# Performance work log

Hardware: AMD Instinct MI355X
Metric: run time of the kernel (lower is better)

## Reference

```python
import jax, jax.numpy as jnp
import numpy as np

B, K, H, W = 16, 32, 28, 28   # batch, set size, image h, image w
HID, OUT = 64, 64             # hid_dim, out_dim
NOPS = 8                      # permutation-equivariant 3->3 pool/broadcast basis ops


def setup_inputs() -> dict:
    key = jax.random.key(0)
    ks = jax.random.split(key, 8)
    def p(k, shape, fan_in):
        return jax.random.normal(k, shape, jnp.float32) / np.float32(np.sqrt(fan_in))
    return dict(
        x=jax.random.normal(ks[0], (B, K, H, W), jnp.float32),
        conv1_w=p(ks[1], (32, 1, 3, 3), 9),
        conv1_b=jnp.zeros((32,), jnp.float32),
        conv2_w=p(ks[2], (64, 32, 3, 3), 32 * 9),
        conv2_b=jnp.zeros((64,), jnp.float32),
        fc_w=p(ks[3], (HID, 64 * 7 * 7), 64 * 7 * 7),
        fc_b=jnp.zeros((HID,), jnp.float32),
        eq_w=p(ks[4], (HID, OUT, NOPS), HID * NOPS),
        eq_b=jnp.zeros((OUT,), jnp.float32),
        out_w=p(ks[5], (1, OUT), OUT),
        out_b=jnp.zeros((1,), jnp.float32),
    )


def _conv2d(x, w, b):
    y = jax.lax.conv_general_dilated(x, w, (1, 1), 'SAME',
                                     dimension_numbers=('NCHW', 'OIHW', 'NCHW'))
    return y + b[None, :, None, None]


def _maxpool2(x):
    return jax.lax.reduce_window(x, -jnp.inf, jax.lax.max,
                                 (1, 1, 2, 2), (1, 1, 2, 2), 'VALID')


def _forward(x, conv1_w, conv1_b, conv2_w, conv2_b, fc_w, fc_b, eq_w, eq_b, out_w, out_b):
    # --- BasicConvNet embed: (B*K, 1, H, W) -> (B*K, HID) ---
    x1 = x.reshape(B * K, 1, H, W)
    h1 = _maxpool2(jax.nn.relu(_conv2d(x1, conv1_w, conv1_b)))   # (B*K, 32, 14, 14)
    h2 = _maxpool2(jax.nn.relu(_conv2d(h1, conv2_w, conv2_b)))   # (B*K, 64, 7, 7)
    feat = jax.nn.relu(h2.reshape(B * K, -1) @ fc_w.T + fc_b)    # (B*K, HID)
    x4 = feat.reshape(B, K, HID)

    # --- triple outer product: (B, HID, K, K, K), no contracted index ---
    x5 = jnp.einsum('bid,bjd,bkd->bdijk', x4, x4, x4)

    # --- SetEq3to3: 8 equivariant pool/broadcast basis ops, contracted with eq_w[d,e,o].
    # Contract each pooled tensor with its slice of eq_w BEFORE broadcasting (same math,
    # avoids materializing 8 full (B,d,K,K,K) op tensors). ---
    m_i  = x5.mean(2)           # (B, d, j, k)
    m_j  = x5.mean(3)           # (B, d, i, k)
    m_k  = x5.mean(4)           # (B, d, i, j)
    m_ij = m_i.mean(2)          # (B, d, k)
    m_ik = m_i.mean(3)          # (B, d, j)
    m_jk = m_j.mean(3)          # (B, d, i)
    m_all = m_ij.mean(2)        # (B, d)

    x6 = (jnp.einsum('bdijk,de->beijk', x5, eq_w[:, :, 0])
          + jnp.einsum('bdjk,de->bejk', m_i, eq_w[:, :, 1])[:, :, None, :, :]
          + jnp.einsum('bdik,de->beik', m_j, eq_w[:, :, 2])[:, :, :, None, :]
          + jnp.einsum('bdij,de->beij', m_k, eq_w[:, :, 3])[:, :, :, :, None]
          + jnp.einsum('bdk,de->bek', m_ij, eq_w[:, :, 4])[:, :, None, None, :]
          + jnp.einsum('bdj,de->bej', m_ik, eq_w[:, :, 5])[:, :, None, :, None]
          + jnp.einsum('bdi,de->bei', m_jk, eq_w[:, :, 6])[:, :, :, None, None]
          + jnp.einsum('bd,de->be', m_all, eq_w[:, :, 7])[:, :, None, None, None]
          + eq_b[None, :, None, None, None])          # (B, OUT, K, K, K)

    # permute to channels-last, relu, pool over (i,j,k), relu, final linear
    x7 = jax.nn.relu(x6.transpose(0, 2, 3, 4, 1))     # (B, K, K, K, OUT)
    x8 = x7.mean(axis=(1, 2, 3))                      # (B, OUT)
    x9 = jax.nn.relu(x8)
    # dropout_prob = 0 -> identity
    return x9 @ out_w.T + out_b                       # (B, 1)


def reference(x, conv1_w, conv1_b, conv2_w, conv2_b, fc_w, fc_b, eq_w, eq_b, out_w, out_b):
    return _forward(x, conv1_w, conv1_b, conv2_w, conv2_b, fc_w, fc_b,
                    eq_w, eq_b, out_w, out_b)
```

## Files before the change

kernel.cpp:

```cpp
#include <hip/hip_runtime.h>
#include <hip/hip_bf16.h>


typedef __attribute__((ext_vector_type(8))) short short8;
typedef __attribute__((ext_vector_type(4))) float f32x4;

__device__ __forceinline__ f32x4 mfma_bf16(short8 a, short8 b, f32x4 c) {
  return __builtin_amdgcn_mfma_f32_16x16x32_bf16(a, b, c, 0, 0, 0);
}

__device__ __forceinline__ unsigned short f2bs(float f) {
  unsigned int u = __float_as_uint(f);
  unsigned int r = u + 0x7fffu + ((u >> 16) & 1u);
  return (unsigned short)(r >> 16);
}
__device__ __forceinline__ unsigned int pk2(float x, float y) {
  union { __hip_bfloat162 h; unsigned int u; } cv;
  cv.h = __float22bfloat162_rn(make_float2(x, y));
  return cv.u;
}
__device__ __forceinline__ void stb4(short* p, float4 v) {
  *(unsigned int*)(p)     = pk2(v.x, v.y);
  *(unsigned int*)(p + 2) = pk2(v.z, v.w);
}

__global__ __launch_bounds__(256) void k1_conv1(const float* __restrict__ x,
    const float* __restrict__ w, const float* __restrict__ bias,
    short* __restrict__ h1b,
    const float* __restrict__ eqw, float* __restrict__ Wt,
    const float* __restrict__ fcw, short* __restrict__ fcwb) {
  const int n = blockIdx.x, t = threadIdx.x;
  if (n >= 512) {
    if (n < 520) {
      const int m = n - 512;
      for (int idx = t; idx < 4096; idx += 256) {
        int e = idx >> 6, d = idx & 63;
        Wt[m*4096 + idx] = eqw[d*512 + e*8 + m];
      }
    } else {
      int base = (n - 520)*12544 + t;
      for (int q = 0; q < 49; ++q) {
        int idx = base + q*256;
        fcwb[idx] = (short)f2bs(fcw[idx]);
      }
    }
    return;
  }
  __shared__ float si[30*30];
  __shared__ float sw[32*9];
  __shared__ float sb[32];
  for (int idx = t; idx < 900; idx += 256) si[idx] = 0.f;
  for (int idx = t; idx < 288; idx += 256) sw[idx] = w[idx];
  if (t < 32) sb[t] = bias[t];
  __syncthreads();
  for (int idx = t; idx < 784; idx += 256) {
    int y = idx / 28, xx = idx - y*28;
    si[(y+1)*30 + xx + 1] = x[n*784 + idx];
  }
  __syncthreads();
  for (int idx = t; idx < 6272; idx += 256) {
    int pos = idx >> 5, c = idx & 31;
    int py = pos / 14, px = pos - py*14;
    float pt[4][4];
#pragma unroll
    for (int r = 0; r < 4; ++r)
#pragma unroll
      for (int q = 0; q < 4; ++q)
        pt[r][q] = si[(2*py + r)*30 + 2*px + q];
    const float* wc = &sw[c*9];
    float w0=wc[0], w1=wc[1], w2=wc[2], w3=wc[3], w4=wc[4], w5=wc[5], w6=wc[6], w7=wc[7], w8=wc[8];
    float bb = sb[c];
    float best = 0.f;
#pragma unroll
    for (int a = 0; a < 2; ++a)
#pragma unroll
      for (int b2 = 0; b2 < 2; ++b2) {
        float v = bb
          + w0*pt[a+0][b2+0] + w1*pt[a+0][b2+1] + w2*pt[a+0][b2+2]
          + w3*pt[a+1][b2+0] + w4*pt[a+1][b2+1] + w5*pt[a+1][b2+2]
          + w6*pt[a+2][b2+0] + w7*pt[a+2][b2+1] + w8*pt[a+2][b2+2];
        best = fmaxf(best, v);
      }
    h1b[n*6272 + idx] = (short)f2bs(best);
  }
}

__global__ __launch_bounds__(256, 2) void k2_mfma(const short* __restrict__ h1b,
    const float* __restrict__ w, const float* __restrict__ bias,
    short* __restrict__ h2b) {
  __shared__ __align__(16) short inT[16*18*40];
  const int n = blockIdx.x, t = threadIdx.x;
  const int wv = t >> 6, l = t & 63, quad = l >> 4, col = l & 15;

  unsigned int* zp = (unsigned int*)inT;
  for (int idx = t; idx < 16*18*20; idx += 256) zp[idx] = 0u;

  const int c_out = wv*16 + col;
  float w72[72];
  {
    const float4* src = (const float4*)(w + c_out*288 + quad*72);
#pragma unroll
    for (int q = 0; q < 18; ++q) {
      float4 v = src[q];
      w72[q*4+0] = v.x; w72[q*4+1] = v.y; w72[q*4+2] = v.z; w72[q*4+3] = v.w;
    }
  }
  union SU { short8 v; unsigned int u[4]; };
  short8 Bq[9];
#pragma unroll
  for (int dd = 0; dd < 9; ++dd) {
    SU b;
#pragma unroll
    for (int q = 0; q < 4; ++q)
      b.u[q] = pk2(w72[(2*q)*9 + dd], w72[(2*q+1)*9 + dd]);
    Bq[dd] = b.v;
  }
  const float bb = bias[c_out];
  __syncthreads();

  {
    const uint4* src = (const uint4*)(h1b + n*6272);
    for (int idx = t; idx < 784; idx += 256) {
      uint4 v = src[idx];
      int pos = idx >> 2, cb = (idx & 3) * 8;
      int y = pos / 14, xx = pos - y*14;
      *(uint4*)&inT[(y+1)*720 + (xx+1)*40 + cb] = v;
    }
  }
  __syncthreads();

  for (int p = 0; p < 7; ++p) {
    short8 Ar[4][3];
#pragma unroll
    for (int rr = 0; rr < 4; ++rr)
#pragma unroll
      for (int dx = 0; dx < 3; ++dx)
        Ar[rr][dx] = *(const short8*)&inT[(2*p + rr)*720 + (col + dx)*40 + quad*8];
    f32x4 a0 = {0.f,0.f,0.f,0.f}, a1 = {0.f,0.f,0.f,0.f};
#pragma unroll
    for (int dy = 0; dy < 3; ++dy)
#pragma unroll
      for (int dx = 0; dx < 3; ++dx) {
        a0 = mfma_bf16(Ar[dy][dx],     Bq[dy*3 + dx], a0);
        a1 = mfma_bf16(Ar[dy + 1][dx], Bq[dy*3 + dx], a1);
      }
#pragma unroll
    for (int a = 0; a < 2; ++a) {
      int px = quad*2 + a;
      if (px < 7) {
        float m0 = fmaxf(fmaxf(a0[2*a], a0[2*a + 1]), fmaxf(a1[2*a], a1[2*a + 1]));
        h2b[n*3136 + c_out*49 + p*7 + px] = (short)f2bs(fmaxf(m0 + bb, 0.f));
      }
    }
  }
}

__global__ __launch_bounds__(256) void k3_mfma(const short* __restrict__ h2b,
    const short* __restrict__ fcwb, float* __restrict__ part) {
  const int blk = blockIdx.x, kp = blockIdx.y, t = threadIdx.x;
  const int w = t >> 6, l = t & 63, quad = l >> 4, col = l & 15;
  const int mt = w & 1, nh = w >> 1;
  const int img = blk*32 + mt*16 + col;
  const short* Ap = h2b + img*3136 + kp*224 + quad*8;
  const short* B0 = fcwb + (nh*32 + col)*3136 + kp*224 + quad*8;
  const short* B1 = fcwb + (nh*32 + 16 + col)*3136 + kp*224 + quad*8;
  f32x4 acc0 = {0.f,0.f,0.f,0.f}, acc1 = {0.f,0.f,0.f,0.f};
#pragma unroll
  for (int q = 0; q < 7; ++q) {
    short8 A  = *(const short8*)(Ap + q*32);
    short8 b0 = *(const short8*)(B0 + q*32);
    short8 b1 = *(const short8*)(B1 + q*32);
    acc0 = mfma_bf16(A, b0, acc0);
    acc1 = mfma_bf16(A, b1, acc1);
  }
  const int e0 = nh*32 + col, e1 = e0 + 16;
  const int base = blk*32 + mt*16 + quad*4;
  float* dst = part + kp*32768;
#pragma unroll
  for (int r = 0; r < 4; ++r) {
    dst[(base + r)*64 + e0] = acc0[r];
    dst[(base + r)*64 + e1] = acc1[r];
  }
}

__global__ __launch_bounds__(256) void k4_prep(const float* __restrict__ part,
    const float* __restrict__ fb, const float* __restrict__ Wt,
    const float* __restrict__ eqb, float* __restrict__ feat,
    float* __restrict__ s, float* __restrict__ t7c, float* __restrict__ x8) {
  __shared__ __align__(16) float sf[2048];
  __shared__ float ss[64];
  const int b = blockIdx.x, t = threadIdx.x;
  for (int v4 = t; v4 < 512; v4 += 256) {
    float4 a = {0.f, 0.f, 0.f, 0.f};
#pragma unroll
    for (int kp = 0; kp < 14; ++kp) {
      float4 p = *(const float4*)&part[kp*32768 + b*2048 + v4*4];
      a.x += p.x; a.y += p.y; a.z += p.z; a.w += p.w;
    }
    float4 fbv = *(const float4*)&fb[(v4*4) & 63];
    float4 r;
    r.x = fmaxf(a.x + fbv.x, 0.f);
    r.y = fmaxf(a.y + fbv.y, 0.f);
    r.z = fmaxf(a.z + fbv.z, 0.f);
    r.w = fmaxf(a.w + fbv.w, 0.f);
    *(float4*)&sf[v4*4] = r;
    *(float4*)&feat[b*2048 + v4*4] = r;
  }
  __syncthreads();
  if (t < 64) {
    float a = 0.f;
    for (int i = 0; i < 32; ++i) a += sf[i*64 + t];
    a *= (1.f/32.f);
    s[b*64 + t] = a;
    ss[t] = a;
  }
  __syncthreads();
  if (t < 64) {
    const float* W7 = Wt + 7*4096 + t*64;
    float t7 = 0.f;
    for (int d = 0; d < 64; ++d) {
      float sv = ss[d];
      t7 += sv*sv*sv * W7[d];
    }
    t7c[b*64 + t] = t7 + eqb[t];
    x8[b*64 + t] = 0.f;
  }
}

__global__ __launch_bounds__(256, 2) void k5_mfma(const float* __restrict__ feat,
    const float* __restrict__ s_, const float* __restrict__ Wt,
    const float* __restrict__ t7c, float* __restrict__ x8) {
  __shared__ __align__(16) float Fm[32*68];
  __shared__ __align__(16) float FI[64];
  __shared__ __align__(16) float SV[64];
  __shared__ __align__(16) float C0[64];
  __shared__ float C0P[128];
  __shared__ float KCf[32*68];
  __shared__ float JCf[32*68];
  __shared__ float RED[256];
  __shared__ __align__(16) short Fb[32*72];
  __shared__ __align__(16) short QPb[64*72];
  __shared__ __align__(16) short G2b[64*72];
  __shared__ __align__(16) short G3b[64*72];

  const int i = blockIdx.x, b = blockIdx.y, t = threadIdx.x;
  const int w = t >> 6, l = t & 63, quad = l >> 4, col = l & 15;

  for (int idx = t; idx < 2048; idx += 256) {
    int r = idx >> 6, d = idx & 63;
    float v = feat[b*2048 + idx];
    Fm[r*68 + d] = v;
    Fb[r*72 + d] = (short)f2bs(v);
  }
  if (t < 64) { FI[t] = feat[b*2048 + i*64 + t]; SV[t] = s_[b*64 + t]; }
  __syncthreads();

  {
    const int e = t >> 2, dbase = (t & 3) * 16;
    const float* W0 = Wt + 0*4096 + e*64;
    const float* W1 = Wt + 1*4096 + e*64;
    const float* W2 = Wt + 2*4096 + e*64;
    const float* W3 = Wt + 3*4096 + e*64;
    const float* W4 = Wt + 4*4096 + e*64;
    const float* W5 = Wt + 5*4096 + e*64;
#pragma unroll
    for (int q = 0; q < 4; ++q) {
      int off = dbase + q*4;
      float4 fi4 = *(const float4*)&FI[off];
      float4 sv4 = *(const float4*)&SV[off];
      float4 w0 = *(const float4*)&W0[off];
      float4 w1 = *(const float4*)&W1[off];
      float4 w2 = *(const float4*)&W2[off];
      float4 w3 = *(const float4*)&W3[off];
      float4 w4 = *(const float4*)&W4[off];
      float4 w5 = *(const float4*)&W5[off];
      float4 qp = fi4*w0 + sv4*w1;
      float4 g2 = sv4*(fi4*w2 + sv4*w4);
      float4 g3 = sv4*(fi4*w3 + sv4*w5);
      stb4(&QPb[e*72 + off], qp);
      stb4(&G2b[e*72 + off], g2);
      stb4(&G3b[e*72 + off], g3);
    }
  }
  if (t < 128) {
    int e = t & 63, dh = t >> 6;
    const float* W6 = Wt + 6*4096 + e*64 + dh*32;
    const float* fip = FI + dh*32;
    const float* svp = SV + dh*32;
    float a = 0.f;
#pragma unroll
    for (int dd = 0; dd < 32; ++dd) {
      float sd = svp[dd];
      a += sd*sd*fip[dd]*W6[dd];
    }
    C0P[dh*64 + e] = a;
  }
  __syncthreads();

  if (w < 2) {
    const short* G = w ? G3b : G2b;
    float* DST = w ? JCf : KCf;
    short8 Bf[4][2];
#pragma unroll
    for (int n = 0; n < 4; ++n)
#pragma unroll
      for (int s2 = 0; s2 < 2; ++s2)
        Bf[n][s2] = *(const short8*)&G[(n*16 + col)*72 + s2*32 + quad*8];
#pragma unroll
    for (int m = 0; m < 2; ++m) {
      short8 A0 = *(const short8*)&Fb[(m*16 + col)*72 + quad*8];
      short8 A1 = *(const short8*)&Fb[(m*16 + col)*72 + 32 + quad*8];
#pragma unroll
      for (int n = 0; n < 4; ++n) {
        f32x4 z = {0.f, 0.f, 0.f, 0.f};
        f32x4 ac = mfma_bf16(A1, Bf[n][1], mfma_bf16(A0, Bf[n][0], z));
#pragma unroll
        for (int r = 0; r < 4; ++r)
          DST[(m*16 + quad*4 + r)*68 + n*16 + col] = ac[r];
      }
    }
  } else if (w == 2) {
    C0[l] = C0P[l] + C0P[64 + l] + t7c[b*64 + l];
  }
  __syncthreads();

  float c0v[4];
#pragma unroll
  for (int n = 0; n < 4; ++n) c0v[n] = C0[n*16 + col];
  float jcq[8][4];
#pragma unroll
  for (int jj = 0; jj < 8; ++jj)
#pragma unroll
    for (int n = 0; n < 4; ++n)
      jcq[jj][n] = JCf[(w*8 + jj)*68 + n*16 + col] + c0v[n];
  float kcv[2][4][4];
#pragma unroll
  for (int kb2 = 0; kb2 < 2; ++kb2)
#pragma unroll
    for (int r = 0; r < 4; ++r)
#pragma unroll
      for (int n = 0; n < 4; ++n)
        kcv[kb2][r][n] = KCf[(kb2*16 + quad*4 + r)*68 + n*16 + col];
  short8 Bq[4][2];
#pragma unroll
  for (int n = 0; n < 4; ++n)
#pragma unroll
    for (int s2 = 0; s2 < 2; ++s2)
      Bq[n][s2] = *(const short8*)&QPb[(n*16 + col)*72 + s2*32 + quad*8];

  float4 fkv[2][4];
#pragma unroll
  for (int kb2 = 0; kb2 < 2; ++kb2) {
    const float* fk = &Fm[(kb2*16 + col)*68 + quad*8];
    fkv[kb2][0] = *(const float4*)(fk);
    fkv[kb2][1] = *(const float4*)(fk + 4);
    fkv[kb2][2] = *(const float4*)(fk + 32);
    fkv[kb2][3] = *(const float4*)(fk + 36);
  }

  float sum[4] = {0.f, 0.f, 0.f, 0.f};
  union SU { short8 v; unsigned int u[4]; };

#pragma unroll
  for (int jj = 0; jj < 8; ++jj) {
    const float* fj = &Fm[(w*8 + jj)*68 + quad*8];
    float4 j0 = *(const float4*)(fj);
    float4 j1 = *(const float4*)(fj + 4);
    float4 j2 = *(const float4*)(fj + 32);
    float4 j3 = *(const float4*)(fj + 36);
#pragma unroll
    for (int kb2 = 0; kb2 < 2; ++kb2) {
      float4 k0 = fkv[kb2][0], k1 = fkv[kb2][1];
      float4 k2v = fkv[kb2][2], k3v = fkv[kb2][3];
      SU A0, A1;
      A0.u[0] = pk2(j0.x*k0.x, j0.y*k0.y);
      A0.u[1] = pk2(j0.z*k0.z, j0.w*k0.w);
      A0.u[2] = pk2(j1.x*k1.x, j1.y*k1.y);
      A0.u[3] = pk2(j1.z*k1.z, j1.w*k1.w);
      A1.u[0] = pk2(j2.x*k2v.x, j2.y*k2v.y);
      A1.u[1] = pk2(j2.z*k2v.z, j2.w*k2v.w);
      A1.u[2] = pk2(j3.x*k3v.x, j3.y*k3v.y);
      A1.u[3] = pk2(j3.z*k3v.z, j3.w*k3v.w);
      f32x4 ac[4];
#pragma unroll
      for (int n = 0; n < 4; ++n) {
        f32x4 z = {0.f, 0.f, 0.f, 0.f};
        ac[n] = mfma_bf16(A1.v, Bq[n][1], mfma_bf16(A0.v, Bq[n][0], z));
      }
#pragma unroll
      for (int n = 0; n < 4; ++n)
#pragma unroll
        for (int r = 0; r < 4; ++r) {
          float v = ac[n][r] + kcv[kb2][r][n] + jcq[jj][n];
          sum[n] += fmaxf(v, 0.f);
        }
    }
  }

#pragma unroll
  for (int n = 0; n < 4; ++n) {
    float v = sum[n];
    v += __shfl_xor(v, 16, 64);
    v += __shfl_xor(v, 32, 64);
    if (l < 16) RED[w*64 + n*16 + l] = v;
  }
  __syncthreads();
  if (t < 64) {
    float tot = RED[t] + RED[64 + t] + RED[128 + t] + RED[192 + t];
    atomicAdd(&x8[b*64 + t], tot);
  }
}

__global__ __launch_bounds__(64) void k6_out(const float* __restrict__ x8,
    const float* __restrict__ ow, const float* __restrict__ ob,
    float* __restrict__ out) {
  const int bb = blockIdx.x, t = threadIdx.x;
  float v = fmaxf(x8[bb*64 + t] * (1.f/32768.f), 0.f) * ow[t];
#pragma unroll
  for (int off = 32; off > 0; off >>= 1) v += __shfl_down(v, off, 64);
  if (t == 0) out[bb] = v + ob[0];
}

extern "C" void kernel_launch(void* const* d_in, const int* in_sizes, int n_in,
                              void* d_out, int out_size, void* d_ws, size_t ws_size,
                              hipStream_t stream) {
  const float* x   = (const float*)d_in[0];
  const float* c1w = (const float*)d_in[1];
  const float* c1b = (const float*)d_in[2];
  const float* c2w = (const float*)d_in[3];
  const float* c2b = (const float*)d_in[4];
  const float* fcw = (const float*)d_in[5];
  const float* fcb = (const float*)d_in[6];
  const float* eqw = (const float*)d_in[7];
  const float* eqb = (const float*)d_in[8];
  const float* ow  = (const float*)d_in[9];
  const float* ob  = (const float*)d_in[10];
  float* out = (float*)d_out;

  short* h1b  = (short*)d_ws;
  short* h2b  = h1b + 512*6272;
  float* feat = (float*)(h2b + 512*3136);
  float* s    = feat + 512*64;
  float* t7c  = s + 1024;
  float* x8   = t7c + 1024;
  float* Wt   = x8 + 1024;
  short* fcwb = (short*)(Wt + 32768);
  float* part = (float*)(fcwb + 200704);

  hipLaunchKernelGGL(k1_conv1, dim3(536), dim3(256), 0, stream,
                     x, c1w, c1b, h1b, eqw, Wt, fcw, fcwb);
  hipLaunchKernelGGL(k2_mfma,  dim3(512), dim3(256), 0, stream, h1b, c2w, c2b, h2b);
  hipLaunchKernelGGL(k3_mfma,  dim3(16, 14), dim3(256), 0, stream, h2b, fcwb, part);
  hipLaunchKernelGGL(k4_prep,  dim3(16),  dim3(256), 0, stream,
                     part, fcb, Wt, eqb, feat, s, t7c, x8);
  hipLaunchKernelGGL(k5_mfma,  dim3(32, 16), dim3(256), 0, stream, feat, s, Wt, t7c, x8);
  hipLaunchKernelGGL(k6_out,   dim3(16),  dim3(64),  0, stream, x8, ow, ob, out);
}
```

Baseline: 131.5 us.

## Fuse conv1 into conv2 kernel and fold output head into k5 via last-block counter

Conv1+relu+pool is computed directly into the shared-memory padded bf16 tile that conv2's MFMA loop reads, so the h1 intermediate no longer goes to global memory and one launch disappears. Conv1 is restructured so each thread computes 4 channels for one pooled position, with weights held in registers and a packed 8-byte shared store. The final output-head kernel is removed: k5 blocks bump a per-batch counter after their atomics, and the last block applies relu and the output linear layer. In exchange the fused kernel carries more registers and shared memory, which may lower occupancy, and the head now depends on the atomic counter and fences.

```diff
diff --git a/kernel.cpp b/kernel.cpp
--- a/kernel.cpp
+++ b/kernel.cpp
@@ -24,9 +24,10 @@
   *(unsigned int*)(p + 2) = pk2(v.z, v.w);
 }
 
-__global__ __launch_bounds__(256) void k1_conv1(const float* __restrict__ x,
-    const float* __restrict__ w, const float* __restrict__ bias,
-    short* __restrict__ h1b,
+__global__ __launch_bounds__(256, 2) void k12_conv(const float* __restrict__ x,
+    const float* __restrict__ w1, const float* __restrict__ b1,
+    const float* __restrict__ w2, const float* __restrict__ b2,
+    short* __restrict__ h2b,
     const float* __restrict__ eqw, float* __restrict__ Wt,
     const float* __restrict__ fcw, short* __restrict__ fcwb) {
   const int n = blockIdx.x, t = threadIdx.x;
@@ -49,82 +50,83 @@
   __shared__ float si[30*30];
   __shared__ float sw[32*9];
   __shared__ float sb[32];
+  __shared__ __align__(16) short inT[16*18*40];
+  const int wv = t >> 6, l = t & 63, quad = l >> 4, col = l & 15;
+
+  const int c_out = wv*16 + col;
+  float w72[72];
+  {
+    const float4* src = (const float4*)(w2 + c_out*288 + quad*72);
+#pragma unroll
+    for (int q = 0; q < 18; ++q) {
+      float4 v = src[q];
+      w72[q*4+0] = v.x; w72[q*4+1] = v.y; w72[q*4+2] = v.z; w72[q*4+3] = v.w;
+    }
+  }
+  union SU { short8 v; unsigned int u[4]; };
+  short8 Bq[9];
+#pragma unroll
+  for (int dd = 0; dd < 9; ++dd) {
+    SU b;
+#pragma unroll
+    for (int q = 0; q < 4; ++q)
+      b.u[q] = pk2(w72[(2*q)*9 + dd], w72[(2*q+1)*9 + dd]);
+    Bq[dd] = b.v;
+  }
+  const float bb2 = b2[c_out];
+
   for (int idx = t; idx < 900; idx += 256) si[idx] = 0.f;
-  for (int idx = t; idx < 288; idx += 256) sw[idx] = w[idx];
-  if (t < 32) sb[t] = bias[t];
+  {
+    unsigned int* zp = (unsigned int*)inT;
+    for (int idx = t; idx < 5760; idx += 256) zp[idx] = 0u;
+  }
+  for (int idx = t; idx < 288; idx += 256) sw[idx] = w1[idx];
+  if (t < 32) sb[t] = b1[t];
   __syncthreads();
   for (int idx = t; idx < 784; idx += 256) {
     int y = idx / 28, xx = idx - y*28;
     si[(y+1)*30 + xx + 1] = x[n*784 + idx];
   }
   __syncthreads();
-  for (int idx = t; idx < 6272; idx += 256) {
-    int pos = idx >> 5, c = idx & 31;
-    int py = pos / 14, px = pos - py*14;
-    float pt[4][4];
-#pragma unroll
-    for (int r = 0; r < 4; ++r)
-#pragma unroll
-      for (int q = 0; q < 4; ++q)
-        pt[r][q] = si[(2*py + r)*30 + 2*px + q];
-    const float* wc = &sw[c*9];
-    float w0=wc[0], w1=wc[1], w2=wc[2], w3=wc[3], w4=wc[4], w5=wc[5], w6=wc[6], w7=wc[7], w8=wc[8];
-    float bb = sb[c];
-    float best = 0.f;
-#pragma unroll
-    for (int a = 0; a < 2; ++a)
-#pragma unroll
-      for (int b2 = 0; b2 < 2; ++b2) {
-        float v = bb
-          + w0*pt[a+0][b2+0] + w1*pt[a+0][b2+1] + w2*pt[a+0][b2+2]
-          + w3*pt[a+1][b2+0] + w4*pt[a+1][b2+1] + w5*pt[a+1][b2+2]
-          + w6*pt[a+2][b2+0] + w7*pt[a+2][b2+1] + w8*pt[a+2][b2+2];
-        best = fmaxf(best, v);
-      }
-    h1b[n*6272 + idx] = (short)f2bs(best);
-  }
-}
-
-__global__ __launch_bounds__(256, 2) void k2_mfma(const short* __restrict__ h1b,
-    const float* __restrict__ w, const float* __restrict__ bias,
-    short* __restrict__ h2b) {
-  __shared__ __align__(16) short inT[16*18*40];
-  const int n = blockIdx.x, t = threadIdx.x;
-  const int wv = t >> 6, l = t & 63, quad = l >> 4, col = l & 15;
-
-  unsigned int* zp = (unsigned int*)inT;
-  for (int idx = t; idx < 16*18*20; idx += 256) zp[idx] = 0u;
-
-  const int c_out = wv*16 + col;
-  float w72[72];
+
   {
-    const float4* src = (const float4*)(w + c_out*288 + quad*72);
-#pragma unroll
-    for (int q = 0; q < 18; ++q) {
-      float4 v = src[q];
-      w72[q*4+0] = v.x; w72[q*4+1] = v.y; w72[q*4+2] = v.z; w72[q*4+3] = v.w;
-    }
-  }
-  union SU { short8 v; unsigned int u[4]; };
-  short8 Bq[9];
-#pragma unroll
-  for (int dd = 0; dd < 9; ++dd) {
-    SU b;
-#pragma unroll
-    for (int q = 0; q < 4; ++q)
-      b.u[q] = pk2(w72[(2*q)*9 + dd], w72[(2*q+1)*9 + dd]);
-    Bq[dd] = b.v;
-  }
-  const float bb = bias[c_out];
-  __syncthreads();
-
-  {
-    const uint4* src = (const uint4*)(h1b + n*6272);
-    for (int idx = t; idx < 784; idx += 256) {
-      uint4 v = src[idx];
-      int pos = idx >> 2, cb = (idx & 3) * 8;
-      int y = pos / 14, xx = pos - y*14;
-      *(uint4*)&inT[(y+1)*720 + (xx+1)*40 + cb] = v;
+    const int cg = t & 7;
+    float wreg[4][9], breg[4];
+#pragma unroll
+    for (int cc = 0; cc < 4; ++cc) {
+      breg[cc] = sb[cg*4 + cc];
+#pragma unroll
+      for (int q = 0; q < 9; ++q) wreg[cc][q] = sw[(cg*4 + cc)*9 + q];
+    }
+    for (int idx = t; idx < 1568; idx += 256) {
+      int pos = idx >> 3;
+      int py = pos / 14, px = pos - py*14;
+      float pt[4][4];
+#pragma unroll
+      for (int r = 0; r < 4; ++r)
+#pragma unroll
+        for (int q = 0; q < 4; ++q)
+          pt[r][q] = si[(2*py + r)*30 + 2*px + q];
+      float res[4];
+#pragma unroll
+      for (int cc = 0; cc < 4; ++cc) {
+        float best = 0.f;
+#pragma unroll
+        for (int a = 0; a < 2; ++a)
+#pragma unroll
+          for (int b3 = 0; b3 < 2; ++b3) {
+            float v = breg[cc]
+              + wreg[cc][0]*pt[a+0][b3+0] + wreg[cc][1]*pt[a+0][b3+1] + wreg[cc][2]*pt[a+0][b3+2]
+              + wreg[cc][3]*pt[a+1][b3+0] + wreg[cc][4]*pt[a+1][b3+1] + wreg[cc][5]*pt[a+1][b3+2]
+              + wreg[cc][6]*pt[a+2][b3+0] + wreg[cc][7]*pt[a+2][b3+1] + wreg[cc][8]*pt[a+2][b3+2];
+            best = fmaxf(best, v);
+          }
+        res[cc] = best;
+      }
+      uint2 pkd;
+      pkd.x = pk2(res[0], res[1]);
+      pkd.y = pk2(res[2], res[3]);
+      *(uint2*)&inT[(py+1)*720 + (px+1)*40 + cg*4] = pkd;
     }
   }
   __syncthreads();
@@ -149,7 +151,7 @@
       int px = quad*2 + a;
       if (px < 7) {
         float m0 = fmaxf(fmaxf(a0[2*a], a0[2*a + 1]), fmaxf(a1[2*a], a1[2*a + 1]));
-        h2b[n*3136 + c_out*49 + p*7 + px] = (short)f2bs(fmaxf(m0 + bb, 0.f));
+        h2b[n*3136 + c_out*49 + p*7 + px] = (short)f2bs(fmaxf(m0 + bb2, 0.f));
       }
     }
   }
@@ -186,7 +188,8 @@
 __global__ __launch_bounds__(256) void k4_prep(const float* __restrict__ part,
     const float* __restrict__ fb, const float* __restrict__ Wt,
     const float* __restrict__ eqb, float* __restrict__ feat,
-    float* __restrict__ s, float* __restrict__ t7c, float* __restrict__ x8) {
+    float* __restrict__ s, float* __restrict__ t7c, float* __restrict__ x8,
+    int* __restrict__ cnt) {
   __shared__ __align__(16) float sf[2048];
   __shared__ float ss[64];
   const int b = blockIdx.x, t = threadIdx.x;
@@ -225,11 +228,14 @@
     t7c[b*64 + t] = t7 + eqb[t];
     x8[b*64 + t] = 0.f;
   }
+  if (t == 0) cnt[b] = 0;
 }
 
 __global__ __launch_bounds__(256, 2) void k5_mfma(const float* __restrict__ feat,
     const float* __restrict__ s_, const float* __restrict__ Wt,
-    const float* __restrict__ t7c, float* __restrict__ x8) {
+    const float* __restrict__ t7c, float* __restrict__ x8, int* __restrict__ cnt,
+    const float* __restrict__ ow, const float* __restrict__ ob,
+    float* __restrict__ out) {
   __shared__ __align__(16) float Fm[32*68];
   __shared__ __align__(16) float FI[64];
   __shared__ __align__(16) float SV[64];
@@ -238,6 +244,7 @@
   __shared__ float KCf[32*68];
   __shared__ float JCf[32*68];
   __shared__ float RED[256];
+  __shared__ int isLast;
   __shared__ __align__(16) short Fb[32*72];
   __shared__ __align__(16) short QPb[64*72];
   __shared__ __align__(16) short G2b[64*72];
@@ -409,16 +416,23 @@
     float tot = RED[t] + RED[64 + t] + RED[128 + t] + RED[192 + t];
     atomicAdd(&x8[b*64 + t], tot);
   }
-}
-
-__global__ __launch_bounds__(64) void k6_out(const float* __restrict__ x8,
-    const float* __restrict__ ow, const float* __restrict__ ob,
-    float* __restrict__ out) {
-  const int bb = blockIdx.x, t = threadIdx.x;
-  float v = fmaxf(x8[bb*64 + t] * (1.f/32768.f), 0.f) * ow[t];
-#pragma unroll
-  for (int off = 32; off > 0; off >>= 1) v += __shfl_down(v, off, 64);
-  if (t == 0) out[bb] = v + ob[0];
+  __syncthreads();
+  if (t == 0) {
+    __threadfence();
+    int old = atomicAdd(&cnt[b], 1);
+    isLast = (old == 31);
+  }
+  __syncthreads();
+  if (isLast) {
+    __threadfence();
+    if (t < 64) {
+      float xv = atomicAdd(&x8[b*64 + t], 0.0f);
+      float v = fmaxf(xv * (1.f/32768.f), 0.f) * ow[t];
+#pragma unroll
+      for (int off = 32; off > 0; off >>= 1) v += __shfl_down(v, off, 64);
+      if (t == 0) out[b] = v + ob[0];
+    }
+  }
 }
 
 extern "C" void kernel_launch(void* const* d_in, const int* in_sizes, int n_in,
@@ -437,22 +451,21 @@
   const float* ob  = (const float*)d_in[10];
   float* out = (float*)d_out;
 
-  short* h1b  = (short*)d_ws;
-  short* h2b  = h1b + 512*6272;
+  short* h2b  = (short*)d_ws;
   float* feat = (float*)(h2b + 512*3136);
   float* s    = feat + 512*64;
   float* t7c  = s + 1024;
   float* x8   = t7c + 1024;
-  float* Wt   = x8 + 1024;
+  int*   cnt  = (int*)(x8 + 1024);
+  float* Wt   = (float*)(cnt + 16);
   short* fcwb = (short*)(Wt + 32768);
   float* part = (float*)(fcwb + 200704);
 
-  hipLaunchKernelGGL(k1_conv1, dim3(536), dim3(256), 0, stream,
-                     x, c1w, c1b, h1b, eqw, Wt, fcw, fcwb);
-  hipLaunchKernelGGL(k2_mfma,  dim3(512), dim3(256), 0, stream, h1b, c2w, c2b, h2b);
+  hipLaunchKernelGGL(k12_conv, dim3(536), dim3(256), 0, stream,
+                     x, c1w, c1b, c2w, c2b, h2b, eqw, Wt, fcw, fcwb);
   hipLaunchKernelGGL(k3_mfma,  dim3(16, 14), dim3(256), 0, stream, h2b, fcwb, part);
   hipLaunchKernelGGL(k4_prep,  dim3(16),  dim3(256), 0, stream,
-                     part, fcb, Wt, eqb, feat, s, t7c, x8);
-  hipLaunchKernelGGL(k5_mfma,  dim3(32, 16), dim3(256), 0, stream, feat, s, Wt, t7c, x8);
-  hipLaunchKernelGGL(k6_out,   dim3(16),  dim3(64),  0, stream, x8, ow, ob, out);
-}
+                     part, fcb, Wt, eqb, feat, s, t7c, x8, cnt);
+  hipLaunchKernelGGL(k5_mfma,  dim3(32, 16), dim3(256), 0, stream,
+                     feat, s, Wt, t7c, x8, cnt, ow, ob, out);
+}
```

Measured after the change: 141.6 us. 1.08x slower.
